# Kernel optimization log

Hardware: AMD Instinct MI355X
Metric: run time of the kernel (lower is better)

The kernel has to match this reference:

```python
import jax, jax.numpy as jnp
import numpy as np

B, S, D, H = 2, 2048, 1024, 16
DK = D // H


def setup_inputs() -> dict:
    key = jax.random.key(0)
    ks = jax.random.split(key, 11)
    std = 1.0 / np.sqrt(D)
    inp = {
        "q": jax.random.normal(ks[0], (B, S, D), jnp.float32),
        "k": jax.random.normal(ks[1], (B, S, D), jnp.float32),
        "v": jax.random.normal(ks[2], (B, S, D), jnp.float32),
        # causal mask, broadcast over batch and heads; masked_fill where mask==0
        "mask": jnp.tril(jnp.ones((S, S), dtype=bool))[None, None, :, :],
        "Wq": jax.random.uniform(ks[3], (D, D), jnp.float32, -std, std),
        "bq": jax.random.uniform(ks[4], (D,), jnp.float32, -std, std),
        "Wk": jax.random.uniform(ks[5], (D, D), jnp.float32, -std, std),
        "bk": jax.random.uniform(ks[6], (D,), jnp.float32, -std, std),
        "Wv": jax.random.uniform(ks[7], (D, D), jnp.float32, -std, std),
        "bv": jax.random.uniform(ks[8], (D,), jnp.float32, -std, std),
        "Wo": jax.random.uniform(ks[9], (D, D), jnp.float32, -std, std),
        "bo": jax.random.uniform(ks[10], (D,), jnp.float32, -std, std),
    }
    return inp


def reference(q, k, v, mask, Wq, bq, Wk, bk, Wv, bv, Wo, bo):
    b, s, _ = q.shape
    # projections, split heads: [B,S,D] -> [B,H,S,dk]
    def proj(x, W, bias):
        return (x @ W + bias).reshape(b, -1, H, DK).transpose(0, 2, 1, 3)
    qh, kh, vh = proj(q, Wq, bq), proj(k, Wk, bk), proj(v, Wv, bv)
    scale = 1.0 / np.sqrt(DK)
    scores = jnp.einsum("bhqd,bhkd->bhqk", qh, kh) * scale  # [B,H,S,S]
    scores = jnp.where(mask, scores, jnp.float32(-1e9))
    attn = jax.nn.softmax(scores, axis=-1)
    out = jnp.einsum("bhqk,bhkd->bhqd", attn, vh)  # [B,H,S,dk]
    concat = out.transpose(0, 2, 1, 3).reshape(b, s, D)
    return concat @ Wo + bo
```

## Files before the change

kernel.cpp:

```cpp
#include <hip/hip_runtime.h>


typedef short v8s  __attribute__((ext_vector_type(8)));
typedef short v4ss __attribute__((ext_vector_type(4)));
typedef float v4f  __attribute__((ext_vector_type(4)));
typedef unsigned int v2u __attribute__((ext_vector_type(2)));

#define S_LEN 2048
#define D_DIM 1024
#define NHEAD 16
#define DK 64
#define M_ROWS 4096

__device__ inline unsigned short f2bf(float f) {
    unsigned x;
    __builtin_memcpy(&x, &f, 4);
    unsigned r = x + 0x7fffu + ((x >> 16) & 1u);
    return (unsigned short)(r >> 16);
}

__device__ inline unsigned cvtpk_bf16(float lo, float hi) {
    unsigned d;
    asm("v_cvt_pk_bf16_f32 %0, %1, %2" : "=v"(d) : "v"(lo), "v"(hi));
    return d;
}

__device__ inline void gload_lds16(const void* g, void* l) {
    __builtin_amdgcn_global_load_lds(
        (const __attribute__((address_space(1))) unsigned int*)g,
        (__attribute__((address_space(3))) unsigned int*)l, 16, 0, 0);
}

__global__ __launch_bounds__(256) void prep(
    const float* __restrict__ q, const float* __restrict__ k,
    const float* __restrict__ v,
    const float* __restrict__ W0, const float* __restrict__ W1,
    const float* __restrict__ W2, const float* __restrict__ W3,
    unsigned short* __restrict__ Xb, unsigned short* __restrict__ Wt)
{
    __shared__ unsigned short t[64][72];
    const int id = blockIdx.x;

    if (id < 6144) {
        const int z = id >> 11;
        const int x = id & 2047;
        const float* X = (z == 0) ? q : (z == 1) ? k : v;
        const size_t off = ((size_t)x * 256 + threadIdx.x) * 8;
        float4 f0 = *(const float4*)(X + off);
        float4 f1 = *(const float4*)(X + off + 4);
        v8s p;
        p[0]=(short)f2bf(f0.x); p[1]=(short)f2bf(f0.y); p[2]=(short)f2bf(f0.z); p[3]=(short)f2bf(f0.w);
        p[4]=(short)f2bf(f1.x); p[5]=(short)f2bf(f1.y); p[6]=(short)f2bf(f1.z); p[7]=(short)f2bf(f1.w);
        *(v8s*)(Xb + (size_t)z * M_ROWS * D_DIM + off) = p;
        return;
    }

    const int tt = id - 6144;
    const int z  = tt >> 8;
    const int rem = tt & 255;
    const int bx = rem & 15;
    const int by = rem >> 4;
    const float* W = (z == 0) ? W0 : (z == 1) ? W1 : (z == 2) ? W2 : W3;
    unsigned short* dst = Wt + (size_t)z * D_DIM * D_DIM;

    const int n0 = bx * 64, k0 = by * 64;
    const int tid = threadIdx.x;
    const int lr = tid >> 4;
    const int lc = (tid & 15) * 4;

#pragma unroll
    for (int kk = 0; kk < 64; kk += 16) {
        float4 f = *(const float4*)(W + (size_t)(k0 + kk + lr) * D_DIM + n0 + lc);
        t[lc + 0][kk + lr] = f2bf(f.x);
        t[lc + 1][kk + lr] = f2bf(f.y);
        t[lc + 2][kk + lr] = f2bf(f.z);
        t[lc + 3][kk + lr] = f2bf(f.w);
    }
    __syncthreads();
    const int wr = tid >> 2;
    const int wc = (tid & 3) * 16;
    v8s o0, o1;
#pragma unroll
    for (int e = 0; e < 8; e++) { o0[e] = t[wr][wc + e]; o1[e] = t[wr][wc + 8 + e]; }
    *(v8s*)(dst + (size_t)(n0 + wr) * D_DIM + k0 + wc)     = o0;
    *(v8s*)(dst + (size_t)(n0 + wr) * D_DIM + k0 + wc + 8) = o1;
}

__global__ __launch_bounds__(256) void gemm_qkv(
    const unsigned short* __restrict__ Xb,
    const unsigned short* __restrict__ Wt,
    const float* __restrict__ bq, const float* __restrict__ bk,
    const float* __restrict__ bv,
    unsigned short* __restrict__ Qp, unsigned short* __restrict__ Kp,
    unsigned short* __restrict__ Vt)
{
    const int id   = blockIdx.x;
    const int xcd  = id & 7;
    const int slot = id >> 3;
    const int nblk = slot & 7;
    const int mg   = (slot >> 3) & 3;
    const int z    = slot >> 5;
    const int mblk = mg * 8 + xcd;

    const unsigned short* X = Xb + (size_t)z * M_ROWS * D_DIM;
    const unsigned short* W = Wt + (size_t)z * D_DIM * D_DIM;
    const float* bias = (z == 0) ? bq : (z == 1) ? bk : bv;

    __shared__ unsigned short lds_a[3][128 * 32];
    __shared__ unsigned short lds_b[3][128 * 32];

    const int tid  = threadIdx.x;
    const int lane = tid & 63;
    const int wave = tid >> 6;
    const int wm   = wave >> 1;
    const int wn   = wave & 1;
    const int quad = lane >> 4;
    const int col  = lane & 15;
    const int m0   = mblk * 128;
    const int n0   = nblk * 128;

    v4f acc[4][4];
#pragma unroll
    for (int i = 0; i < 4; i++)
#pragma unroll
        for (int j = 0; j < 4; j++)
#pragma unroll
            for (int r = 0; r < 4; r++) acc[i][j][r] = 0.0f;

    const int srow = wave * 16 + (lane >> 2);
    const int schk = (lane & 3) * 8;
    const int soff = wave * 512 + lane * 8;

    const unsigned short* Xr0 = X + (size_t)(m0 + srow) * D_DIM + schk;
    const unsigned short* Xr1 = X + (size_t)(m0 + 64 + srow) * D_DIM + schk;
    const unsigned short* Wr0 = W + (size_t)(n0 + srow) * D_DIM + schk;
    const unsigned short* Wr1 = W + (size_t)(n0 + 64 + srow) * D_DIM + schk;

    auto stage = [&](unsigned short* A, unsigned short* B, int k0) {
        gload_lds16(Xr0 + k0, A + soff);
        gload_lds16(Xr1 + k0, A + soff + 2048);
        gload_lds16(Wr0 + k0, B + soff);
        gload_lds16(Wr1 + k0, B + soff + 2048);
    };

    auto compute = [&](const unsigned short* A, const unsigned short* B) {
        v8s af[4], bf[4];
#pragma unroll
        for (int mt = 0; mt < 4; mt++)
            af[mt] = *(const v8s*)(A + (wm * 64 + mt * 16 + col) * 32 + quad * 8);
#pragma unroll
        for (int nt = 0; nt < 4; nt++)
            bf[nt] = *(const v8s*)(B + (wn * 64 + nt * 16 + col) * 32 + quad * 8);
#pragma unroll
        for (int mt = 0; mt < 4; mt++)
#pragma unroll
            for (int nt = 0; nt < 4; nt++)
                acc[mt][nt] = __builtin_amdgcn_mfma_f32_16x16x32_bf16(
                    af[mt], bf[nt], acc[mt][nt], 0, 0, 0);
    };

    stage(lds_a[0], lds_b[0], 0);
    stage(lds_a[1], lds_b[1], 32);

    unsigned short *ra = lds_a[0], *rb = lds_b[0];
    unsigned short *pa = lds_a[1], *pb = lds_b[1];
    unsigned short *sa = lds_a[2], *sb = lds_b[2];

    for (int k0 = 0; k0 < 992; k0 += 32) {
        asm volatile("s_waitcnt vmcnt(4)" ::: "memory");
        asm volatile("s_waitcnt lgkmcnt(0)" ::: "memory");
        __builtin_amdgcn_sched_barrier(0);
        __builtin_amdgcn_s_barrier();
        __builtin_amdgcn_sched_barrier(0);
        if (k0 + 64 < 1024) stage(sa, sb, k0 + 64);
        compute(ra, rb);
        unsigned short* t;
        t = ra; ra = pa; pa = sa; sa = t;
        t = rb; rb = pb; pb = sb; sb = t;
    }
    asm volatile("s_waitcnt vmcnt(0)" ::: "memory");
    asm volatile("s_waitcnt lgkmcnt(0)" ::: "memory");
    __builtin_amdgcn_sched_barrier(0);
    __builtin_amdgcn_s_barrier();
    __builtin_amdgcn_sched_barrier(0);
    compute(ra, rb);

    int   nn[4];
    float bvv[4];
#pragma unroll
    for (int nt = 0; nt < 4; nt++) {
        nn[nt]  = n0 + wn * 64 + nt * 16 + col;
        bvv[nt] = bias[nn[nt]];
    }

    if (z < 2) {
        unsigned short* out = (z == 0) ? Qp : Kp;
#pragma unroll
        for (int mt = 0; mt < 4; mt++) {
#pragma unroll
            for (int nt = 0; nt < 4; nt++) {
                const int h  = nn[nt] >> 6;
                const int dk = nn[nt] & 63;
#pragma unroll
                for (int r = 0; r < 4; r++) {
                    int row = m0 + wm * 64 + mt * 16 + quad * 4 + r;
                    int b   = row >> 11, t = row & 2047;
                    out[(((size_t)(b * NHEAD + h) * S_LEN) + t) * DK + dk] =
                        f2bf(acc[mt][nt][r] + bvv[nt]);
                }
            }
        }
    } else {
#pragma unroll
        for (int mt = 0; mt < 4; mt++) {
#pragma unroll
            for (int nt = 0; nt < 4; nt++) {
                const int h  = nn[nt] >> 6;
                const int dk = nn[nt] & 63;
                int row = m0 + wm * 64 + mt * 16 + quad * 4;
                int b   = row >> 11, t = row & 2047;
                v4ss pk;
#pragma unroll
                for (int r = 0; r < 4; r++) pk[r] = (short)f2bf(acc[mt][nt][r] + bvv[nt]);
                *(v4ss*)(Vt + ((size_t)(b * NHEAD + h) * DK + dk) * S_LEN + t) = pk;
            }
        }
    }
}

__global__ __launch_bounds__(128) void flash12(
    const unsigned short* __restrict__ Qp,
    const unsigned short* __restrict__ Kp,
    const unsigned short* __restrict__ Vt,
    unsigned short* __restrict__ Op)
{
    __shared__ __align__(16) unsigned char smem[18432];

    const int tid  = threadIdx.x;
    const int wave = tid >> 6;
    const int lane = tid & 63;
    const int quad = lane >> 4;
    const int col  = lane & 15;

    unsigned short* pwA = (unsigned short*)smem + wave * 2 * (32 * 72);
    unsigned short* pwB = pwA + 32 * 72;

    const int i   = blockIdx.x;
    const int xcd = i & 7;
    const int j   = i >> 3;
    const int bh  = xcd * 4 + (j & 3);
    const int pr  = j >> 2;
    const int q32a = 63 - pr, q32b = pr;
    const int r0a = q32a * 32, r0b = q32b * 32;
    const int nsA = (q32a >> 1) + 1;
    const int nsB = (q32b >> 1) + 1;

    const unsigned short* Qh = Qp + (size_t)bh * S_LEN * DK;
    const unsigned short* Kh = Kp + (size_t)bh * S_LEN * DK;
    const unsigned short* Vh = Vt + (size_t)bh * DK * S_LEN;

    v8s qfa[2][2], qfb[2][2];
#pragma unroll
    for (int mt = 0; mt < 2; mt++)
#pragma unroll
        for (int c = 0; c < 2; c++) {
            qfa[mt][c] = *(const v8s*)(Qh + (size_t)(r0a + mt * 16 + col) * DK + c * 32 + quad * 8);
            qfb[mt][c] = *(const v8s*)(Qh + (size_t)(r0b + mt * 16 + col) * DK + c * 32 + quad * 8);
        }

    float lpa[2] = {0.f, 0.f}, lpb[2] = {0.f, 0.f};
    v4f acca[2][4], accb[2][4];
#pragma unroll
    for (int mt = 0; mt < 2; mt++)
#pragma unroll
        for (int nt = 0; nt < 4; nt++)
#pragma unroll
            for (int r = 0; r < 4; r++) { acca[mt][nt][r] = 0.0f; accb[mt][nt][r] = 0.0f; }

    const float CS = 0.18033688f;
    const float CM = 28.8539008f;

    v8s kc[2][4];
    const int kvp = wave * 64;
#pragma unroll
    for (int c = 0; c < 2; c++)
#pragma unroll
        for (int nt = 0; nt < 4; nt++)
            kc[c][nt] = *(const v8s*)(Kh + (size_t)(kvp + nt * 16 + col) * DK + c * 32 + quad * 8);

    for (int step = wave; step < nsA; step += 2) {
        const int kv0 = step * 64;
        const int kvn = (step + 2 < nsA) ? kv0 + 128 : kv0;
        const bool doB = (step < nsB);

        v8s vf[2][4];
#pragma unroll
        for (int c = 0; c < 2; c++)
#pragma unroll
            for (int nt = 0; nt < 4; nt++)
                vf[c][nt] = *(const v8s*)(Vh + (size_t)(nt * 16 + col) * S_LEN + kv0 + c * 32 + quad * 8);
        v8s kn[2][4];
#pragma unroll
        for (int c = 0; c < 2; c++)
#pragma unroll
            for (int nt = 0; nt < 4; nt++)
                kn[c][nt] = *(const v8s*)(Kh + (size_t)(kvn + nt * 16 + col) * DK + c * 32 + quad * 8);

#pragma unroll
        for (int mt = 0; mt < 2; mt++) {
            v4f s[4];
            __builtin_amdgcn_s_setprio(1);
#pragma unroll
            for (int nt = 0; nt < 4; nt++) {
#pragma unroll
                for (int r = 0; r < 4; r++) s[nt][r] = 0.0f;
#pragma unroll
                for (int c = 0; c < 2; c++)
                    s[nt] = __builtin_amdgcn_mfma_f32_16x16x32_bf16(kc[c][nt], qfa[mt][c], s[nt], 0, 0, 0);
            }
            __builtin_amdgcn_s_setprio(0);

            const int rbase = r0a + mt * 16;
            float lp = 0.f;
            if (kv0 + 64 > rbase) {
#pragma unroll
                for (int nt = 0; nt < 4; nt++)
#pragma unroll
                    for (int r = 0; r < 4; r++) {
                        float p = __builtin_amdgcn_exp2f(fmaf(s[nt][r], CS, -CM));
                        if (kv0 + nt * 16 + quad * 4 + r > rbase + col) p = 0.0f;
                        s[nt][r] = p;
                        lp += p;
                    }
            } else {
#pragma unroll
                for (int nt = 0; nt < 4; nt++)
#pragma unroll
                    for (int r = 0; r < 4; r++) {
                        float p = __builtin_amdgcn_exp2f(fmaf(s[nt][r], CS, -CM));
                        s[nt][r] = p;
                        lp += p;
                    }
            }
            lpa[mt] += lp;

#pragma unroll
            for (int nt = 0; nt < 4; nt++) {
                unsigned u0 = cvtpk_bf16(s[nt][0], s[nt][1]);
                unsigned u1 = cvtpk_bf16(s[nt][2], s[nt][3]);
                v2u w; w[0] = u0; w[1] = u1;
                *(v2u*)(pwA + (mt * 16 + col) * 72 + nt * 16 + quad * 4) = w;
            }
        }

        if (doB) {
#pragma unroll
            for (int mt = 0; mt < 2; mt++) {
                v4f s[4];
                __builtin_amdgcn_s_setprio(1);
#pragma unroll
                for (int nt = 0; nt < 4; nt++) {
#pragma unroll
                    for (int r = 0; r < 4; r++) s[nt][r] = 0.0f;
#pragma unroll
                    for (int c = 0; c < 2; c++)
                        s[nt] = __builtin_amdgcn_mfma_f32_16x16x32_bf16(kc[c][nt], qfb[mt][c], s[nt], 0, 0, 0);
                }
                __builtin_amdgcn_s_setprio(0);

                const int rbase = r0b + mt * 16;
                float lp = 0.f;
                if (kv0 + 64 > rbase) {
#pragma unroll
                    for (int nt = 0; nt < 4; nt++)
#pragma unroll
                        for (int r = 0; r < 4; r++) {
                            float p = __builtin_amdgcn_exp2f(fmaf(s[nt][r], CS, -CM));
                            if (kv0 + nt * 16 + quad * 4 + r > rbase + col) p = 0.0f;
                            s[nt][r] = p;
                            lp += p;
                        }
                } else {
#pragma unroll
                    for (int nt = 0; nt < 4; nt++)
#pragma unroll
                        for (int r = 0; r < 4; r++) {
                            float p = __builtin_amdgcn_exp2f(fmaf(s[nt][r], CS, -CM));
                            s[nt][r] = p;
                            lp += p;
                        }
                }
                lpb[mt] += lp;

#pragma unroll
                for (int nt = 0; nt < 4; nt++) {
                    unsigned u0 = cvtpk_bf16(s[nt][0], s[nt][1]);
                    unsigned u1 = cvtpk_bf16(s[nt][2], s[nt][3]);
                    v2u w; w[0] = u0; w[1] = u1;
                    *(v2u*)(pwB + (mt * 16 + col) * 72 + nt * 16 + quad * 4) = w;
                }
            }
        }

        __builtin_amdgcn_s_setprio(1);
#pragma unroll
        for (int mt = 0; mt < 2; mt++)
#pragma unroll
            for (int c = 0; c < 2; c++) {
                v8s af = *(const v8s*)(pwA + (mt * 16 + col) * 72 + c * 32 + quad * 8);
#pragma unroll
                for (int nt = 0; nt < 4; nt++)
                    acca[mt][nt] = __builtin_amdgcn_mfma_f32_16x16x32_bf16(af, vf[c][nt], acca[mt][nt], 0, 0, 0);
            }
        if (doB) {
#pragma unroll
            for (int mt = 0; mt < 2; mt++)
#pragma unroll
                for (int c = 0; c < 2; c++) {
                    v8s af = *(const v8s*)(pwB + (mt * 16 + col) * 72 + c * 32 + quad * 8);
#pragma unroll
                    for (int nt = 0; nt < 4; nt++)
                        accb[mt][nt] = __builtin_amdgcn_mfma_f32_16x16x32_bf16(af, vf[c][nt], accb[mt][nt], 0, 0, 0);
                }
        }
        __builtin_amdgcn_s_setprio(0);

#pragma unroll
        for (int c = 0; c < 2; c++)
#pragma unroll
            for (int nt = 0; nt < 4; nt++)
                kc[c][nt] = kn[c][nt];
    }

#pragma unroll
    for (int mt = 0; mt < 2; mt++) {
        lpa[mt] += __shfl_xor(lpa[mt], 16);
        lpa[mt] += __shfl_xor(lpa[mt], 32);
        lpb[mt] += __shfl_xor(lpb[mt], 16);
        lpb[mt] += __shfl_xor(lpb[mt], 32);
    }

    float* comb = (float*)smem;
    __syncthreads();
    if (wave == 1) {
        float* dst = comb + lane * 68;
#pragma unroll
        for (int mt = 0; mt < 2; mt++)
#pragma unroll
            for (int nt = 0; nt < 4; nt++) {
                *(v4f*)(dst + (mt * 4 + nt) * 4)      = acca[mt][nt];
                *(v4f*)(dst + 34 + (mt * 4 + nt) * 4) = accb[mt][nt];
            }
        dst[32] = lpa[0]; dst[33] = lpa[1];
        dst[66] = lpb[0]; dst[67] = lpb[1];
    }
    __syncthreads();
    if (wave != 0) return;

    {
        const float* src = comb + lane * 68;
#pragma unroll
        for (int mt = 0; mt < 2; mt++)
#pragma unroll
            for (int nt = 0; nt < 4; nt++) {
                v4f oa = *(const v4f*)(src + (mt * 4 + nt) * 4);
                v4f ob = *(const v4f*)(src + 34 + (mt * 4 + nt) * 4);
#pragma unroll
                for (int r = 0; r < 4; r++) { acca[mt][nt][r] += oa[r]; accb[mt][nt][r] += ob[r]; }
            }
        lpa[0] += src[32]; lpa[1] += src[33];
        lpb[0] += src[66]; lpb[1] += src[67];
    }

    lpa[0] = 1.0f / lpa[0];  lpa[1] = 1.0f / lpa[1];
    lpb[0] = 1.0f / lpb[0];  lpb[1] = 1.0f / lpb[1];
    float lia[2][4], lib[2][4];
#pragma unroll
    for (int mt = 0; mt < 2; mt++)
#pragma unroll
        for (int r = 0; r < 4; r++) {
            lia[mt][r] = __shfl(lpa[mt], quad * 4 + r);
            lib[mt][r] = __shfl(lpb[mt], quad * 4 + r);
        }

#pragma unroll
    for (int mt = 0; mt < 2; mt++) {
#pragma unroll
        for (int nt = 0; nt < 4; nt++) {
#pragma unroll
            for (int r = 0; r < 4; r++) {
                size_t aA = ((size_t)bh * S_LEN + r0a + mt * 16 + quad * 4 + r) * DK + nt * 16 + col;
                Op[aA] = f2bf(acca[mt][nt][r] * lia[mt][r]);
                size_t aB = ((size_t)bh * S_LEN + r0b + mt * 16 + quad * 4 + r) * DK + nt * 16 + col;
                Op[aB] = f2bf(accb[mt][nt][r] * lib[mt][r]);
            }
        }
    }
}

__global__ __launch_bounds__(256) void gemm_out(
    const unsigned short* __restrict__ Ap,
    const unsigned short* __restrict__ Wot,
    const float* __restrict__ bo,
    float* __restrict__ out)
{
    __shared__ unsigned short lds_a[3][64 * 32];
    __shared__ unsigned short lds_b[3][128 * 32];

    const int id   = blockIdx.x;
    const int xcd  = id & 7;
    const int slot = id >> 3;
    const int nblk = slot & 7;
    const int mg   = slot >> 3;
    const int mblk = mg * 8 + xcd;

    const int tid  = threadIdx.x;
    const int lane = tid & 63;
    const int wave = tid >> 6;
    const int wm   = wave >> 1;
    const int wn   = wave & 1;
    const int quad = lane >> 4;
    const int col  = lane & 15;
    const int m0   = mblk * 64;
    const int n0   = nblk * 128;

    v4f acc[2][4];
#pragma unroll
    for (int i = 0; i < 2; i++)
#pragma unroll
        for (int j = 0; j < 4; j++)
#pragma unroll
            for (int r = 0; r < 4; r++) acc[i][j][r] = 0.0f;

    const int srow = wave * 16 + (lane >> 2);
    const int schk = (lane & 3) * 8;
    const int soff = wave * 512 + lane * 8;

    const int tokA = m0 + srow;
    const int bbA  = tokA >> 11, ttA = tokA & 2047;
    const unsigned short* Abase = Ap + ((size_t)bbA * NHEAD * S_LEN + ttA) * DK;
    const unsigned short* Wr0 = Wot + (size_t)(n0 + srow) * D_DIM + schk;
    const unsigned short* Wr1 = Wot + (size_t)(n0 + 64 + srow) * D_DIM + schk;

    auto stage = [&](unsigned short* A, unsigned short* B, int k0) {
        const int h_  = k0 >> 6;
        const int dk_ = (k0 & 63) + schk;
        gload_lds16(Abase + (size_t)h_ * S_LEN * DK + dk_, A + soff);
        gload_lds16(Wr0 + k0, B + soff);
        gload_lds16(Wr1 + k0, B + soff + 2048);
    };

    auto compute = [&](const unsigned short* A, const unsigned short* B) {
        v8s af[2], bf[4];
#pragma unroll
        for (int mt = 0; mt < 2; mt++)
            af[mt] = *(const v8s*)(A + (wm * 32 + mt * 16 + col) * 32 + quad * 8);
#pragma unroll
        for (int nt = 0; nt < 4; nt++)
            bf[nt] = *(const v8s*)(B + (wn * 64 + nt * 16 + col) * 32 + quad * 8);
#pragma unroll
        for (int mt = 0; mt < 2; mt++)
#pragma unroll
            for (int nt = 0; nt < 4; nt++)
                acc[mt][nt] = __builtin_amdgcn_mfma_f32_16x16x32_bf16(
                    af[mt], bf[nt], acc[mt][nt], 0, 0, 0);
    };

    stage(lds_a[0], lds_b[0], 0);
    stage(lds_a[1], lds_b[1], 32);

    unsigned short *ra = lds_a[0], *rb = lds_b[0];
    unsigned short *pa = lds_a[1], *pb = lds_b[1];
    unsigned short *sa = lds_a[2], *sb = lds_b[2];

    for (int k0 = 0; k0 < 992; k0 += 32) {
        asm volatile("s_waitcnt vmcnt(3)" ::: "memory");
        asm volatile("s_waitcnt lgkmcnt(0)" ::: "memory");
        __builtin_amdgcn_sched_barrier(0);
        __builtin_amdgcn_s_barrier();
        __builtin_amdgcn_sched_barrier(0);
        if (k0 + 64 < 1024) stage(sa, sb, k0 + 64);
        compute(ra, rb);
        unsigned short* t;
        t = ra; ra = pa; pa = sa; sa = t;
        t = rb; rb = pb; pb = sb; sb = t;
    }
    asm volatile("s_waitcnt vmcnt(0)" ::: "memory");
    asm volatile("s_waitcnt lgkmcnt(0)" ::: "memory");
    __builtin_amdgcn_sched_barrier(0);
    __builtin_amdgcn_s_barrier();
    __builtin_amdgcn_sched_barrier(0);
    compute(ra, rb);

    float bvv[4];
    int   nn[4];
#pragma unroll
    for (int nt = 0; nt < 4; nt++) {
        nn[nt]  = n0 + wn * 64 + nt * 16 + col;
        bvv[nt] = bo[nn[nt]];
    }

#pragma unroll
    for (int mt = 0; mt < 2; mt++) {
#pragma unroll
        for (int nt = 0; nt < 4; nt++) {
#pragma unroll
            for (int r = 0; r < 4; r++) {
                int row = m0 + wm * 32 + mt * 16 + quad * 4 + r;
                out[(size_t)row * D_DIM + nn[nt]] = acc[mt][nt][r] + bvv[nt];
            }
        }
    }
}

extern "C" void kernel_launch(void* const* d_in, const int* in_sizes, int n_in,
                              void* d_out, int out_size, void* d_ws, size_t ws_size,
                              hipStream_t stream) {
    const float* q  = (const float*)d_in[0];
    const float* k  = (const float*)d_in[1];
    const float* v  = (const float*)d_in[2];
    const float* Wq = (const float*)d_in[4];
    const float* bq = (const float*)d_in[5];
    const float* Wk = (const float*)d_in[6];
    const float* bk = (const float*)d_in[7];
    const float* Wv = (const float*)d_in[8];
    const float* bv = (const float*)d_in[9];
    const float* Wo = (const float*)d_in[10];
    const float* bo = (const float*)d_in[11];
    float* out = (float*)d_out;

    unsigned short* ws = (unsigned short*)d_ws;
    const size_t WT   = (size_t)D_DIM * D_DIM;
    const size_t TENS = (size_t)M_ROWS * D_DIM;
    unsigned short* Wt = ws;
    unsigned short* Qp = ws + 4 * WT;
    unsigned short* Kp = Qp + TENS;
    unsigned short* Vt = Kp + TENS;
    unsigned short* Xb = Vt + TENS;
    unsigned short* Ap = Xb;

    prep<<<7168, 256, 0, stream>>>(q, k, v, Wq, Wk, Wv, Wo, Xb, Wt);
    gemm_qkv<<<768, 256, 0, stream>>>(Xb, Wt, bq, bk, bv, Qp, Kp, Vt);
    flash12<<<1024, 128, 0, stream>>>(Qp, Kp, Vt, Ap);
    gemm_out<<<512, 256, 0, stream>>>(Ap, Wt + 3 * WT, bo, out);
}
```

Baseline: 237.1 us.

## Halve GEMM N-tiles and switch to simple double-buffered LDS pipeline

Both projection GEMMs now use 64-wide N tiles instead of 128, which doubles the grid to 1536 and 1024 blocks and halves per-block accumulators and LDS. The triple-buffered pipeline with manual waitcnt and barriers is replaced by a plain double-buffered loop using __syncthreads. The aim is higher occupancy and more blocks to fill the CUs. In exchange, arithmetic intensity drops because A tiles are reloaded for twice as many N blocks, and the simpler sync exposes more load latency.

```diff
diff --git a/kernel.cpp b/kernel.cpp
--- a/kernel.cpp
+++ b/kernel.cpp
@@ -97,17 +97,17 @@
     const int id   = blockIdx.x;
     const int xcd  = id & 7;
     const int slot = id >> 3;
-    const int nblk = slot & 7;
-    const int mg   = (slot >> 3) & 3;
-    const int z    = slot >> 5;
+    const int nblk = slot & 15;
+    const int mg   = (slot >> 4) & 3;
+    const int z    = slot >> 6;
     const int mblk = mg * 8 + xcd;
 
     const unsigned short* X = Xb + (size_t)z * M_ROWS * D_DIM;
     const unsigned short* W = Wt + (size_t)z * D_DIM * D_DIM;
     const float* bias = (z == 0) ? bq : (z == 1) ? bk : bv;
 
-    __shared__ unsigned short lds_a[3][128 * 32];
-    __shared__ unsigned short lds_b[3][128 * 32];
+    __shared__ unsigned short lds_a[2][128 * 32];
+    __shared__ unsigned short lds_b[2][64 * 32];
 
     const int tid  = threadIdx.x;
     const int lane = tid & 63;
@@ -117,13 +117,13 @@
     const int quad = lane >> 4;
     const int col  = lane & 15;
     const int m0   = mblk * 128;
-    const int n0   = nblk * 128;
-
-    v4f acc[4][4];
+    const int n0   = nblk * 64;
+
+    v4f acc[4][2];
 #pragma unroll
     for (int i = 0; i < 4; i++)
 #pragma unroll
-        for (int j = 0; j < 4; j++)
+        for (int j = 0; j < 2; j++)
 #pragma unroll
             for (int r = 0; r < 4; r++) acc[i][j][r] = 0.0f;
 
@@ -134,62 +134,45 @@
     const unsigned short* Xr0 = X + (size_t)(m0 + srow) * D_DIM + schk;
     const unsigned short* Xr1 = X + (size_t)(m0 + 64 + srow) * D_DIM + schk;
     const unsigned short* Wr0 = W + (size_t)(n0 + srow) * D_DIM + schk;
-    const unsigned short* Wr1 = W + (size_t)(n0 + 64 + srow) * D_DIM + schk;
-
-    auto stage = [&](unsigned short* A, unsigned short* B, int k0) {
-        gload_lds16(Xr0 + k0, A + soff);
-        gload_lds16(Xr1 + k0, A + soff + 2048);
-        gload_lds16(Wr0 + k0, B + soff);
-        gload_lds16(Wr1 + k0, B + soff + 2048);
+
+    auto stage = [&](int buf, int k0) {
+        gload_lds16(Xr0 + k0, lds_a[buf] + soff);
+        gload_lds16(Xr1 + k0, lds_a[buf] + soff + 2048);
+        gload_lds16(Wr0 + k0, lds_b[buf] + soff);
     };
 
-    auto compute = [&](const unsigned short* A, const unsigned short* B) {
-        v8s af[4], bf[4];
+    auto compute = [&](int buf) {
+        v8s af[4], bf[2];
 #pragma unroll
         for (int mt = 0; mt < 4; mt++)
-            af[mt] = *(const v8s*)(A + (wm * 64 + mt * 16 + col) * 32 + quad * 8);
-#pragma unroll
-        for (int nt = 0; nt < 4; nt++)
-            bf[nt] = *(const v8s*)(B + (wn * 64 + nt * 16 + col) * 32 + quad * 8);
+            af[mt] = *(const v8s*)(lds_a[buf] + (wm * 64 + mt * 16 + col) * 32 + quad * 8);
+#pragma unroll
+        for (int nt = 0; nt < 2; nt++)
+            bf[nt] = *(const v8s*)(lds_b[buf] + (wn * 32 + nt * 16 + col) * 32 + quad * 8);
 #pragma unroll
         for (int mt = 0; mt < 4; mt++)
 #pragma unroll
-            for (int nt = 0; nt < 4; nt++)
+            for (int nt = 0; nt < 2; nt++)
                 acc[mt][nt] = __builtin_amdgcn_mfma_f32_16x16x32_bf16(
                     af[mt], bf[nt], acc[mt][nt], 0, 0, 0);
     };
 
-    stage(lds_a[0], lds_b[0], 0);
-    stage(lds_a[1], lds_b[1], 32);
-
-    unsigned short *ra = lds_a[0], *rb = lds_b[0];
-    unsigned short *pa = lds_a[1], *pb = lds_b[1];
-    unsigned short *sa = lds_a[2], *sb = lds_b[2];
-
-    for (int k0 = 0; k0 < 992; k0 += 32) {
-        asm volatile("s_waitcnt vmcnt(4)" ::: "memory");
-        asm volatile("s_waitcnt lgkmcnt(0)" ::: "memory");
-        __builtin_amdgcn_sched_barrier(0);
-        __builtin_amdgcn_s_barrier();
-        __builtin_amdgcn_sched_barrier(0);
-        if (k0 + 64 < 1024) stage(sa, sb, k0 + 64);
-        compute(ra, rb);
-        unsigned short* t;
-        t = ra; ra = pa; pa = sa; sa = t;
-        t = rb; rb = pb; pb = sb; sb = t;
-    }
-    asm volatile("s_waitcnt vmcnt(0)" ::: "memory");
-    asm volatile("s_waitcnt lgkmcnt(0)" ::: "memory");
-    __builtin_amdgcn_sched_barrier(0);
-    __builtin_amdgcn_s_barrier();
-    __builtin_amdgcn_sched_barrier(0);
-    compute(ra, rb);
-
-    int   nn[4];
-    float bvv[4];
-#pragma unroll
-    for (int nt = 0; nt < 4; nt++) {
-        nn[nt]  = n0 + wn * 64 + nt * 16 + col;
+    stage(0, 0);
+    __syncthreads();
+
+    int cur = 0;
+    for (int k0 = 0; k0 < D_DIM; k0 += 32) {
+        if (k0 + 32 < D_DIM) stage(cur ^ 1, k0 + 32);
+        compute(cur);
+        __syncthreads();
+        cur ^= 1;
+    }
+
+    int   nn[2];
+    float bvv[2];
+#pragma unroll
+    for (int nt = 0; nt < 2; nt++) {
+        nn[nt]  = n0 + wn * 32 + nt * 16 + col;
         bvv[nt] = bias[nn[nt]];
     }
 
@@ -198,7 +181,7 @@
 #pragma unroll
         for (int mt = 0; mt < 4; mt++) {
 #pragma unroll
-            for (int nt = 0; nt < 4; nt++) {
+            for (int nt = 0; nt < 2; nt++) {
                 const int h  = nn[nt] >> 6;
                 const int dk = nn[nt] & 63;
 #pragma unroll
@@ -214,7 +197,7 @@
 #pragma unroll
         for (int mt = 0; mt < 4; mt++) {
 #pragma unroll
-            for (int nt = 0; nt < 4; nt++) {
+            for (int nt = 0; nt < 2; nt++) {
                 const int h  = nn[nt] >> 6;
                 const int dk = nn[nt] & 63;
                 int row = m0 + wm * 64 + mt * 16 + quad * 4;
@@ -504,14 +487,14 @@
     const float* __restrict__ bo,
     float* __restrict__ out)
 {
-    __shared__ unsigned short lds_a[3][64 * 32];
-    __shared__ unsigned short lds_b[3][128 * 32];
+    __shared__ unsigned short lds_a[2][64 * 32];
+    __shared__ unsigned short lds_b[2][64 * 32];
 
     const int id   = blockIdx.x;
     const int xcd  = id & 7;
     const int slot = id >> 3;
-    const int nblk = slot & 7;
-    const int mg   = slot >> 3;
+    const int nblk = slot & 15;
+    const int mg   = slot >> 4;
     const int mblk = mg * 8 + xcd;
 
     const int tid  = threadIdx.x;
@@ -522,13 +505,13 @@
     const int quad = lane >> 4;
     const int col  = lane & 15;
     const int m0   = mblk * 64;
-    const int n0   = nblk * 128;
-
-    v4f acc[2][4];
+    const int n0   = nblk * 64;
+
+    v4f acc[2][2];
 #pragma unroll
     for (int i = 0; i < 2; i++)
 #pragma unroll
-        for (int j = 0; j < 4; j++)
+        for (int j = 0; j < 2; j++)
 #pragma unroll
             for (int r = 0; r < 4; r++) acc[i][j][r] = 0.0f;
 
@@ -540,70 +523,53 @@
     const int bbA  = tokA >> 11, ttA = tokA & 2047;
     const unsigned short* Abase = Ap + ((size_t)bbA * NHEAD * S_LEN + ttA) * DK;
     const unsigned short* Wr0 = Wot + (size_t)(n0 + srow) * D_DIM + schk;
-    const unsigned short* Wr1 = Wot + (size_t)(n0 + 64 + srow) * D_DIM + schk;
-
-    auto stage = [&](unsigned short* A, unsigned short* B, int k0) {
+
+    auto stage = [&](int buf, int k0) {
         const int h_  = k0 >> 6;
         const int dk_ = (k0 & 63) + schk;
-        gload_lds16(Abase + (size_t)h_ * S_LEN * DK + dk_, A + soff);
-        gload_lds16(Wr0 + k0, B + soff);
-        gload_lds16(Wr1 + k0, B + soff + 2048);
+        gload_lds16(Abase + (size_t)h_ * S_LEN * DK + dk_, lds_a[buf] + soff);
+        gload_lds16(Wr0 + k0, lds_b[buf] + soff);
     };
 
-    auto compute = [&](const unsigned short* A, const unsigned short* B) {
-        v8s af[2], bf[4];
+    auto compute = [&](int buf) {
+        v8s af[2], bf[2];
 #pragma unroll
         for (int mt = 0; mt < 2; mt++)
-            af[mt] = *(const v8s*)(A + (wm * 32 + mt * 16 + col) * 32 + quad * 8);
-#pragma unroll
-        for (int nt = 0; nt < 4; nt++)
-            bf[nt] = *(const v8s*)(B + (wn * 64 + nt * 16 + col) * 32 + quad * 8);
+            af[mt] = *(const v8s*)(lds_a[buf] + (wm * 32 + mt * 16 + col) * 32 + quad * 8);
+#pragma unroll
+        for (int nt = 0; nt < 2; nt++)
+            bf[nt] = *(const v8s*)(lds_b[buf] + (wn * 32 + nt * 16 + col) * 32 + quad * 8);
 #pragma unroll
         for (int mt = 0; mt < 2; mt++)
 #pragma unroll
-            for (int nt = 0; nt < 4; nt++)
+            for (int nt = 0; nt < 2; nt++)
                 acc[mt][nt] = __builtin_amdgcn_mfma_f32_16x16x32_bf16(
                     af[mt], bf[nt], acc[mt][nt], 0, 0, 0);
     };
 
-    stage(lds_a[0], lds_b[0], 0);
-    stage(lds_a[1], lds_b[1], 32);
-
-    unsigned short *ra = lds_a[0], *rb = lds_b[0];
-    unsigned short *pa = lds_a[1], *pb = lds_b[1];
-    unsigned short *sa = lds_a[2], *sb = lds_b[2];
-
-    for (int k0 = 0; k0 < 992; k0 += 32) {
-        asm volatile("s_waitcnt vmcnt(3)" ::: "memory");
-        asm volatile("s_waitcnt lgkmcnt(0)" ::: "memory");
-        __builtin_amdgcn_sched_barrier(0);
-        __builtin_amdgcn_s_barrier();
-        __builtin_amdgcn_sched_barrier(0);
-        if (k0 + 64 < 1024) stage(sa, sb, k0 + 64);
-        compute(ra, rb);
-        unsigned short* t;
-        t = ra; ra = pa; pa = sa; sa = t;
-        t = rb; rb = pb; pb = sb; sb = t;
-    }
-    asm volatile("s_waitcnt vmcnt(0)" ::: "memory");
-    asm volatile("s_waitcnt lgkmcnt(0)" ::: "memory");
-    __builtin_amdgcn_sched_barrier(0);
-    __builtin_amdgcn_s_barrier();
-    __builtin_amdgcn_sched_barrier(0);
-    compute(ra, rb);
-
-    float bvv[4];
-    int   nn[4];
-#pragma unroll
-    for (int nt = 0; nt < 4; nt++) {
-        nn[nt]  = n0 + wn * 64 + nt * 16 + col;
+    stage(0, 0);
+    __syncthreads();
+
+    int cur = 0;
+    for (int k0 = 0; k0 < D_DIM; k0 += 32) {
+        if (k0 + 32 < D_DIM) stage(cur ^ 1, k0 + 32);
+        compute(cur);
+        __syncthreads();
+        cur ^= 1;
+    }
+
+    float bvv[2];
+    int   nn[2];
+#pragma unroll
+    for (int nt = 0; nt < 2; nt++) {
+        nn[nt]  = n0 + wn * 32 + nt * 16 + col;
         bvv[nt] = bo[nn[nt]];
     }
 
 #pragma unroll
     for (int mt = 0; mt < 2; mt++) {
 #pragma unroll
-        for (int nt = 0; nt < 4; nt++) {
+        for (int nt = 0; nt < 2; nt++) {
 #pragma unroll
             for (int r = 0; r < 4; r++) {
                 int row = m0 + wm * 32 + mt * 16 + quad * 4 + r;
@@ -640,7 +606,7 @@
     unsigned short* Ap = Xb;
 
     prep<<<7168, 256, 0, stream>>>(q, k, v, Wq, Wk, Wv, Wo, Xb, Wt);
-    gemm_qkv<<<768, 256, 0, stream>>>(Xb, Wt, bq, bk, bv, Qp, Kp, Vt);
+    gemm_qkv<<<1536, 256, 0, stream>>>(Xb, Wt, bq, bk, bv, Qp, Kp, Vt);
     flash12<<<1024, 128, 0, stream>>>(Qp, Kp, Vt, Ap);
-    gemm_out<<<512, 256, 0, stream>>>(Ap, Wt + 3 * WT, bo, out);
-}
+    gemm_out<<<1024, 256, 0, stream>>>(Ap, Wt + 3 * WT, bo, out);
+}
```

Measured after the change: 255.8 us. +7.9%, slower.
